# Kernel tuning notes

Hardware: AMD Instinct MI355X
Metric: run time of the kernel (lower is better)

## Reference

```python
import jax, jax.numpy as jnp
import numpy as np

B, A, EMBED, HIDDEN, PROJ = 256, 16, 1024, 1024, 256


def setup_inputs() -> dict:
    key = jax.random.key(0)
    k0, k1, k2 = jax.random.split(key, 3)
    return {
        "agent_embeddings": jax.random.normal(k0, (B, A, EMBED), dtype=jnp.float32),
        "w1": jax.random.normal(k1, (EMBED, HIDDEN), dtype=jnp.float32) * (1.0 / np.sqrt(EMBED)),
        "b1": jnp.zeros((HIDDEN,), dtype=jnp.float32),
        "w2": jax.random.normal(k2, (HIDDEN, PROJ), dtype=jnp.float32) * (1.0 / np.sqrt(HIDDEN)),
        "b2": jnp.zeros((PROJ,), dtype=jnp.float32),
        "log_scale": jnp.asarray(0.0, dtype=jnp.float32),  # log(init_logit_scale=1.0)
        "logit_bias": jnp.asarray(0.0, dtype=jnp.float32),
    }


def reference(agent_embeddings, w1, b1, w2, b2, log_scale, logit_bias):
    b, a, d = agent_embeddings.shape
    n = b * a
    x = agent_embeddings.reshape(n, d)
    # MLP projector: Linear -> GELU (exact, torch default) -> [dropout=identity at eval] -> Linear
    h = jax.nn.gelu(x @ w1 + b1, approximate=False)
    p = h @ w2 + b2  # [N, proj_dim]
    z = p / jnp.linalg.norm(p, axis=-1, keepdims=True)
    # cosine similarity logits, scaled + biased
    logits = (z @ z.T) * jnp.exp(log_scale) + logit_bias  # [N, N]
    # block-diagonal labels: 1 iff same batch element
    ids = jnp.arange(n) // a
    m1 = jnp.where(ids[:, None] == ids[None, :], 1.0, -1.0)  # 2*labels - 1
    loglik = jax.nn.log_sigmoid(m1 * logits)
    loss = jnp.mean(-jnp.sum(loglik, axis=-1))
    embeddings = z.reshape(b, a, -1)
    return embeddings, loss, logits
```

## Files before the change

### kernel.cpp

```cpp
#include <hip/hip_runtime.h>
#include <math.h>


#define NTOK 4096
#define DEMB 1024
#define DHID 1024
#define DPRJ 256

typedef __attribute__((ext_vector_type(8))) short bf16x8;
typedef __attribute__((ext_vector_type(4))) float f32x4;

typedef __attribute__((address_space(3))) void lds_void_t;
typedef __attribute__((address_space(1))) const void gbl_void_t;

static __device__ __forceinline__ void glds16(const void* g, void* l) {
    __builtin_amdgcn_global_load_lds((gbl_void_t*)g, (lds_void_t*)l, 16, 0, 0);
}

static __device__ __forceinline__ void split2(float v, ushort* h, ushort* l) {
    const uint u = __float_as_uint(v);
    *h = (ushort)(u >> 16);
    const float r = v - __uint_as_float(u & 0xffff0000u);
    *l = (ushort)(__float_as_uint(r) >> 16);
}
static __device__ __forceinline__ float gelu_fast(float v) {
    const float x  = v * 0.70710678118654752440f;
    const float ax = fabsf(x);
    const float t  = 1.0f / (1.0f + 0.3275911f * ax);
    const float poly = t * (0.254829592f + t * (-0.284496736f + t * (1.421413741f
                     + t * (-1.453152027f + t * 1.061405429f))));
    const float erf_ax = 1.0f - poly * __expf(-ax * ax);
    return 0.5f * v * (1.0f + copysignf(erf_ax, x));
}
static __device__ __forceinline__ float log_sigmoid_fast(float x) {
    return fminf(x, 0.0f) - __logf(1.0f + __expf(-fabsf(x)));
}

__global__ __launch_bounds__(256)
void k_cvt_T(const float* __restrict__ W, ushort* __restrict__ WtH,
             ushort* __restrict__ WtL, int K, int N)
{
    __shared__ float tile[32][33];
    const int tn0 = blockIdx.x * 32;
    const int tk0 = blockIdx.y * 32;
    const int tr = threadIdx.x >> 5;
    const int tc = threadIdx.x & 31;
#pragma unroll
    for (int p = 0; p < 4; ++p)
        tile[tr + 8 * p][tc] = W[(size_t)(tk0 + tr + 8 * p) * N + tn0 + tc];
    __syncthreads();
#pragma unroll
    for (int p = 0; p < 4; ++p) {
        const int n = tr + 8 * p;
        ushort h, l;
        split2(tile[tc][n], &h, &l);
        WtH[(size_t)(tn0 + n) * K + tk0 + tc] = h;
        WtL[(size_t)(tn0 + n) * K + tk0 + tc] = l;
    }
}

__global__ __launch_bounds__(256)
void k_cvt_X(const float* __restrict__ X, ushort* __restrict__ Xh,
             ushort* __restrict__ Xl)
{
    const size_t idx = ((size_t)blockIdx.x * 256 + threadIdx.x) * 8;
    const float4 v0 = *(const float4*)(X + idx);
    const float4 v1 = *(const float4*)(X + idx + 4);
    const float vv[8] = {v0.x, v0.y, v0.z, v0.w, v1.x, v1.y, v1.z, v1.w};
    uint4 hv, lv;
#pragma unroll
    for (int e = 0; e < 8; ++e)
        split2(vv[e], (ushort*)&hv + e, (ushort*)&lv + e);
    *(uint4*)(Xh + idx) = hv;
    *(uint4*)(Xl + idx) = lv;
}

__global__ __launch_bounds__(512, 1)
void k_gemm1(const ushort* __restrict__ Xh, const ushort* __restrict__ Xl,
             const ushort* __restrict__ W1tH, const ushort* __restrict__ W1tL,
             const float* __restrict__ B1, int bm0,
             ushort* __restrict__ Hh, ushort* __restrict__ Hl)
{
    __shared__ __align__(16) ushort sm[49152];
    ushort* Ah = sm;
    ushort* Al = sm + 16384;
    ushort* Bh = sm + 32768;
    ushort* Bl = sm + 40960;

    const int t = threadIdx.x, lane = t & 63, w = t >> 6;
    const int wr = w >> 2, wc = w & 3;
    const int bmr = blockIdx.x * 128;
    const int bn  = blockIdx.y * 64;
    const int kb = lane >> 4, lr = lane & 15;

    f32x4 acc[4];
#pragma unroll
    for (int i = 0; i < 4; ++i) acc[i] = (f32x4){0.f, 0.f, 0.f, 0.f};

    for (int ph = 0; ph < 8; ++ph) {
        const int ko = ph * 128;
        if (ph) __syncthreads();
#pragma unroll
        for (int q = 0; q < 4; ++q) {
            const int row = w * 16 + q * 4 + (lane >> 4);
            const int gck = (lane & 15) ^ (row & 15);
            const size_t ga = (size_t)(bmr + row) * DEMB + ko + (gck << 3);
            const int lo = (w * 16 + q * 4) * 128;
            glds16(Xh + ga, Ah + lo);
            glds16(Xl + ga, Al + lo);
        }
#pragma unroll
        for (int q = 0; q < 2; ++q) {
            const int row = w * 8 + q * 4 + (lane >> 4);
            const int gck = (lane & 15) ^ (row & 15);
            const size_t gb = (size_t)(bn + row) * DEMB + ko + (gck << 3);
            const int lo = (w * 8 + q * 4) * 128;
            glds16(W1tH + gb, Bh + lo);
            glds16(W1tL + gb, Bl + lo);
        }
        __syncthreads();
#pragma unroll
        for (int ks = 0; ks < 4; ++ks) {
            const int g = ks * 4 + kb;
            const int colL = wc * 16 + lr;
            const int ob = colL * 128 + ((g ^ (colL & 15)) << 3);
            const bf16x8 bh = *(const bf16x8*)(Bh + ob);
            const bf16x8 bl = *(const bf16x8*)(Bl + ob);
#pragma unroll
            for (int i = 0; i < 4; ++i) {
                const int rowL = wr * 64 + i * 16 + lr;
                const int oa = rowL * 128 + ((g ^ (rowL & 15)) << 3);
                const bf16x8 ah = *(const bf16x8*)(Ah + oa);
                const bf16x8 al = *(const bf16x8*)(Al + oa);
                acc[i] = __builtin_amdgcn_mfma_f32_16x16x32_bf16(ah, bh, acc[i], 0, 0, 0);
                acc[i] = __builtin_amdgcn_mfma_f32_16x16x32_bf16(ah, bl, acc[i], 0, 0, 0);
                acc[i] = __builtin_amdgcn_mfma_f32_16x16x32_bf16(al, bh, acc[i], 0, 0, 0);
            }
        }
    }

    const int col = bn + wc * 16 + lr;
    const float b = B1[col];
#pragma unroll
    for (int i = 0; i < 4; ++i) {
#pragma unroll
        for (int e = 0; e < 4; ++e) {
            const int row = bm0 + bmr + wr * 64 + i * 16 + kb * 4 + e;
            const float g = gelu_fast(acc[i][e] + b);
            ushort h, l;
            split2(g, &h, &l);
            Hh[(size_t)row * DHID + col] = h;
            Hl[(size_t)row * DHID + col] = l;
        }
    }
}

__global__ __launch_bounds__(512, 1)
void k_gemm2(const ushort* __restrict__ Hh, const ushort* __restrict__ Hl,
             const ushort* __restrict__ W2tH, const ushort* __restrict__ W2tL,
             float* __restrict__ P)
{
    __shared__ __align__(16) ushort sm[49152];
    ushort* Ah = sm;
    ushort* Al = sm + 16384;
    ushort* Bh = sm + 32768;
    ushort* Bl = sm + 40960;

    const int t = threadIdx.x, lane = t & 63, w = t >> 6;
    const int wr = w >> 2, wc = w & 3;
    const int bmr = blockIdx.x * 128;
    const int bn  = blockIdx.y * 64;
    const int k0  = blockIdx.z * 512;
    const int kb = lane >> 4, lr = lane & 15;

    f32x4 acc[4];
#pragma unroll
    for (int i = 0; i < 4; ++i) acc[i] = (f32x4){0.f, 0.f, 0.f, 0.f};

    for (int ph = 0; ph < 4; ++ph) {
        const int ko = k0 + ph * 128;
        if (ph) __syncthreads();
#pragma unroll
        for (int q = 0; q < 4; ++q) {
            const int row = w * 16 + q * 4 + (lane >> 4);
            const int gck = (lane & 15) ^ (row & 15);
            const size_t ga = (size_t)(bmr + row) * DHID + ko + (gck << 3);
            const int lo = (w * 16 + q * 4) * 128;
            glds16(Hh + ga, Ah + lo);
            glds16(Hl + ga, Al + lo);
        }
#pragma unroll
        for (int q = 0; q < 2; ++q) {
            const int row = w * 8 + q * 4 + (lane >> 4);
            const int gck = (lane & 15) ^ (row & 15);
            const size_t gb = (size_t)(bn + row) * DHID + ko + (gck << 3);
            const int lo = (w * 8 + q * 4) * 128;
            glds16(W2tH + gb, Bh + lo);
            glds16(W2tL + gb, Bl + lo);
        }
        __syncthreads();
#pragma unroll
        for (int ks = 0; ks < 4; ++ks) {
            const int g = ks * 4 + kb;
            const int colL = wc * 16 + lr;
            const int ob = colL * 128 + ((g ^ (colL & 15)) << 3);
            const bf16x8 bh = *(const bf16x8*)(Bh + ob);
            const bf16x8 bl = *(const bf16x8*)(Bl + ob);
#pragma unroll
            for (int i = 0; i < 4; ++i) {
                const int rowL = wr * 64 + i * 16 + lr;
                const int oa = rowL * 128 + ((g ^ (rowL & 15)) << 3);
                const bf16x8 ah = *(const bf16x8*)(Ah + oa);
                const bf16x8 al = *(const bf16x8*)(Al + oa);
                acc[i] = __builtin_amdgcn_mfma_f32_16x16x32_bf16(ah, bh, acc[i], 0, 0, 0);
                acc[i] = __builtin_amdgcn_mfma_f32_16x16x32_bf16(ah, bl, acc[i], 0, 0, 0);
                acc[i] = __builtin_amdgcn_mfma_f32_16x16x32_bf16(al, bh, acc[i], 0, 0, 0);
            }
        }
    }

    float* Pz = P + (size_t)blockIdx.z * NTOK * DPRJ;
    const int col = bn + wc * 16 + lr;
#pragma unroll
    for (int i = 0; i < 4; ++i) {
#pragma unroll
        for (int e = 0; e < 4; ++e) {
            const int row = bmr + wr * 64 + i * 16 + kb * 4 + e;
            Pz[(size_t)row * DPRJ + col] = acc[i][e];
        }
    }
}

__global__ __launch_bounds__(256)
void k_norm(const float* __restrict__ P, const float* __restrict__ B2,
            float* __restrict__ Zo, ushort* __restrict__ Zbh,
            ushort* __restrict__ Zbl)
{
    const int r = blockIdx.x;
    const int c = threadIdx.x;

    const float v = P[(size_t)r * DPRJ + c]
                  + P[(size_t)NTOK * DPRJ + (size_t)r * DPRJ + c] + B2[c];
    float ss = v * v;
#pragma unroll
    for (int o = 32; o > 0; o >>= 1) ss += __shfl_down(ss, o);
    __shared__ float wsum[4];
    if ((c & 63) == 0) wsum[c >> 6] = ss;
    __syncthreads();
    const float tot = wsum[0] + wsum[1] + wsum[2] + wsum[3];
    const float z = v / sqrtf(tot);
    Zo[(size_t)r * DPRJ + c] = z;
    ushort h, l;
    split2(z, &h, &l);
    Zbh[(size_t)r * DPRJ + c] = h;
    Zbl[(size_t)r * DPRJ + c] = l;
}

__global__ __launch_bounds__(512, 1)
void k_gemm3(const ushort* __restrict__ Zbh, const ushort* __restrict__ Zbl,
             const float* __restrict__ LS, const float* __restrict__ LB,
             float* __restrict__ Lg, float* __restrict__ partial)
{
    __shared__ __align__(16) ushort sm[65536];
    ushort* Ah = sm;
    ushort* Al = sm + 16384;
    ushort* Bh = sm + 32768;
    ushort* Bl = sm + 49152;

    const int t = threadIdx.x, lane = t & 63, w = t >> 6;
    const int wr = w >> 2, wc = w & 3;
    const int bm = blockIdx.x * 128, bn = blockIdx.y * 128;
    const int kb = lane >> 4, lr = lane & 15;
    const int srow0 = w * 16;

    f32x4 acc[4][2];
#pragma unroll
    for (int i = 0; i < 4; ++i)
#pragma unroll
        for (int j = 0; j < 2; ++j) acc[i][j] = (f32x4){0.f, 0.f, 0.f, 0.f};

    float lsum = 0.0f;

#pragma unroll
    for (int ph = 0; ph < 2; ++ph) {
        const int ko = ph * 128;
        if (ph) __syncthreads();
#pragma unroll
        for (int q = 0; q < 4; ++q) {
            const int row = srow0 + q * 4 + (lane >> 4);
            const int gck = (lane & 15) ^ (row & 15);
            const size_t ga = (size_t)(bm + row) * DPRJ + ko + (gck << 3);
            const size_t gb = (size_t)(bn + row) * DPRJ + ko + (gck << 3);
            const int lo = (srow0 + q * 4) * 128;
            glds16(Zbh + ga, Ah + lo);
            glds16(Zbl + ga, Al + lo);
            glds16(Zbh + gb, Bh + lo);
            glds16(Zbl + gb, Bl + lo);
        }
        __syncthreads();
#pragma unroll
        for (int ks = 0; ks < 4; ++ks) {
            const int g = ks * 4 + kb;
            bf16x8 bhf[2], blf[2];
#pragma unroll
            for (int j = 0; j < 2; ++j) {
                const int col = wc * 32 + j * 16 + lr;
                const int o = col * 128 + ((g ^ (col & 15)) << 3);
                bhf[j] = *(const bf16x8*)(Bh + o);
                blf[j] = *(const bf16x8*)(Bl + o);
            }
#pragma unroll
            for (int i = 0; i < 4; ++i) {
                const int row = wr * 64 + i * 16 + lr;
                const int o = row * 128 + ((g ^ (row & 15)) << 3);
                const bf16x8 ah = *(const bf16x8*)(Ah + o);
                const bf16x8 al = *(const bf16x8*)(Al + o);
#pragma unroll
                for (int j = 0; j < 2; ++j) {
                    acc[i][j] = __builtin_amdgcn_mfma_f32_16x16x32_bf16(ah, bhf[j], acc[i][j], 0, 0, 0);
                    acc[i][j] = __builtin_amdgcn_mfma_f32_16x16x32_bf16(ah, blf[j], acc[i][j], 0, 0, 0);
                    acc[i][j] = __builtin_amdgcn_mfma_f32_16x16x32_bf16(al, bhf[j], acc[i][j], 0, 0, 0);
                }
            }
        }
    }

    const float scale = __expf(LS[0]);
    const float lbias = LB[0];

    __syncthreads();
    float* fT = (float*)sm;
#pragma unroll
    for (int j = 0; j < 2; ++j) {
        const int col = bn + wc * 32 + j * 16 + lr;
        const int cid = col >> 4;
#pragma unroll
        for (int i = 0; i < 4; ++i) {
#pragma unroll
            for (int e = 0; e < 4; ++e) {
                const int rloc = wr * 64 + i * 16 + kb * 4 + e;
                const float lg = fmaf(acc[i][j][e], scale, lbias);
                fT[rloc * 132 + (wc * 32 + j * 16 + lr)] = lg;
                const float x = (((bm + rloc) >> 4) == cid) ? lg : -lg;
                lsum += log_sigmoid_fast(x);
            }
        }
    }
    __syncthreads();

#pragma unroll
    for (int q = 0; q < 32; ++q) {
        const int e = q * 512 + t;
        const int row = e >> 7, c = e & 127;
        Lg[(size_t)(bm + row) * NTOK + bn + c] = fT[row * 132 + c];
    }

#pragma unroll
    for (int o = 32; o > 0; o >>= 1) lsum += __shfl_down(lsum, o);
    __shared__ float wsum[8];
    if (lane == 0) wsum[w] = lsum;
    __syncthreads();
    if (t == 0) {
        float s = 0.f;
#pragma unroll
        for (int i = 0; i < 8; ++i) s += wsum[i];
        partial[blockIdx.y * gridDim.x + blockIdx.x] = s;
    }
}

__global__ __launch_bounds__(256)
void k_finalize(const float* __restrict__ partial, float* __restrict__ loss_out)
{
    const int t = threadIdx.x;
    double s = (double)partial[t] + (double)partial[t + 256]
             + (double)partial[t + 512] + (double)partial[t + 768];
#pragma unroll
    for (int o = 32; o > 0; o >>= 1) s += __shfl_down(s, o);
    __shared__ double ws4[4];
    if ((t & 63) == 0) ws4[t >> 6] = s;
    __syncthreads();
    if (t == 0)
        loss_out[0] = (float)(-(ws4[0] + ws4[1] + ws4[2] + ws4[3]) / (double)NTOK);
}

extern "C" void kernel_launch(void* const* d_in, const int* in_sizes, int n_in,
                              void* d_out, int out_size, void* d_ws, size_t ws_size,
                              hipStream_t stream)
{
    const float* X  = (const float*)d_in[0];
    const float* W1 = (const float*)d_in[1];
    const float* B1 = (const float*)d_in[2];
    const float* W2 = (const float*)d_in[3];
    const float* B2 = (const float*)d_in[4];
    const float* LS = (const float*)d_in[5];
    const float* LB = (const float*)d_in[6];

    float* out  = (float*)d_out;
    float* Zo   = out;
    float* loss = out + (size_t)NTOK * DPRJ;
    float* Lg   = loss + 1;

    char* ws = (char*)d_ws;
    ushort* Hh   = (ushort*)(ws);
    ushort* Hl   = (ushort*)(ws + 8388608);
    ushort* Xsh  = (ushort*)(ws + 16777216);
    ushort* Xsl  = (ushort*)(ws + 20971520);
    float*  P    = (float*) (ws + 16777216);
    ushort* W1tH = (ushort*)(ws + 25165824);
    ushort* W1tL = (ushort*)(ws + 27262976);
    ushort* Zbh  = (ushort*)(ws + 25165824);
    ushort* Zbl  = (ushort*)(ws + 27262976);
    ushort* W2tH = (ushort*)(ws + 29360128);
    ushort* W2tL = (ushort*)(ws + 29884416);
    float*  part = (float*) (ws + 30408704);

    k_cvt_T <<<dim3(32, 32),   256, 0, stream>>>(W1, W1tH, W1tL, DEMB, DHID);
    k_cvt_T <<<dim3(8, 32),    256, 0, stream>>>(W2, W2tH, W2tL, DHID, DPRJ);
    k_cvt_X <<<dim3(1024),     256, 0, stream>>>(X, Xsh, Xsl);
    k_gemm1 <<<dim3(16, 16),   512, 0, stream>>>(Xsh, Xsl, W1tH, W1tL, B1, 0, Hh, Hl);
    k_cvt_X <<<dim3(1024),     256, 0, stream>>>(X + (size_t)2048 * DEMB, Xsh, Xsl);
    k_gemm1 <<<dim3(16, 16),   512, 0, stream>>>(Xsh, Xsl, W1tH, W1tL, B1, 2048, Hh, Hl);

    k_gemm2 <<<dim3(32, 4, 2), 512, 0, stream>>>(Hh, Hl, W2tH, W2tL, P);
    k_norm  <<<dim3(4096),     256, 0, stream>>>(P, B2, Zo, Zbh, Zbl);
    k_gemm3 <<<dim3(32, 32),   512, 0, stream>>>(Zbh, Zbl, LS, LB, Lg, part);
    k_finalize<<<1, 256, 0, stream>>>(part, loss);
}
```

Baseline: 208.1 us.

## Double-buffer GEMM1/GEMM2 LDS stages, shrink K tiles, raise occupancy, merge weight conversion

GEMM1 and GEMM2 switch from single-buffered 128-wide K stages to double-buffered 64-wide stages, so the global-to-LDS loads for the next stage can overlap the MFMA work on the current one. The LDS footprint per block stays the same, and launch bounds now allow two blocks per CU. GEMM3 uses 64-wide K stages with half the LDS and four blocks per CU, and writes logits out through LDS in two halves. The two weight conversion launches become a single kernel. The risks are more barriers per K step and higher register pressure under the tighter launch bounds.

```diff
diff --git a/kernel.cpp b/kernel.cpp
--- a/kernel.cpp
+++ b/kernel.cpp
@@ -37,12 +37,23 @@
 }
 
 __global__ __launch_bounds__(256)
-void k_cvt_T(const float* __restrict__ W, ushort* __restrict__ WtH,
-             ushort* __restrict__ WtL, int K, int N)
+void k_cvt_W(const float* __restrict__ W1, ushort* __restrict__ W1tH,
+             ushort* __restrict__ W1tL, const float* __restrict__ W2,
+             ushort* __restrict__ W2tH, ushort* __restrict__ W2tL)
 {
     __shared__ float tile[32][33];
-    const int tn0 = blockIdx.x * 32;
-    const int tk0 = blockIdx.y * 32;
+    int id = blockIdx.x;
+    const float* W;
+    ushort *WtH, *WtL;
+    int K, N, tn0, tk0;
+    if (id < 1024) {
+        W = W1; WtH = W1tH; WtL = W1tL; K = DEMB; N = DHID;
+        tn0 = (id & 31) * 32; tk0 = (id >> 5) * 32;
+    } else {
+        id -= 1024;
+        W = W2; WtH = W2tH; WtL = W2tL; K = DHID; N = DPRJ;
+        tn0 = (id & 7) * 32; tk0 = (id >> 3) * 32;
+    }
     const int tr = threadIdx.x >> 5;
     const int tc = threadIdx.x & 31;
 #pragma unroll
@@ -75,68 +86,71 @@
     *(uint4*)(Xl + idx) = lv;
 }
 
-__global__ __launch_bounds__(512, 1)
+#define G1B 24576
+__global__ __launch_bounds__(512, 2)
 void k_gemm1(const ushort* __restrict__ Xh, const ushort* __restrict__ Xl,
              const ushort* __restrict__ W1tH, const ushort* __restrict__ W1tL,
              const float* __restrict__ B1, int bm0,
              ushort* __restrict__ Hh, ushort* __restrict__ Hl)
 {
-    __shared__ __align__(16) ushort sm[49152];
-    ushort* Ah = sm;
-    ushort* Al = sm + 16384;
-    ushort* Bh = sm + 32768;
-    ushort* Bl = sm + 40960;
-
+    __shared__ __align__(16) ushort sm[2 * G1B];
     const int t = threadIdx.x, lane = t & 63, w = t >> 6;
     const int wr = w >> 2, wc = w & 3;
-    const int bmr = blockIdx.x * 128;
-    const int bn  = blockIdx.y * 64;
+    const int bmr = blockIdx.x * 128, bn = blockIdx.y * 64;
     const int kb = lane >> 4, lr = lane & 15;
+    const int srow = lane >> 3, sck = lane & 7;
 
     f32x4 acc[4];
 #pragma unroll
     for (int i = 0; i < 4; ++i) acc[i] = (f32x4){0.f, 0.f, 0.f, 0.f};
 
-    for (int ph = 0; ph < 8; ++ph) {
-        const int ko = ph * 128;
-        if (ph) __syncthreads();
-#pragma unroll
-        for (int q = 0; q < 4; ++q) {
-            const int row = w * 16 + q * 4 + (lane >> 4);
-            const int gck = (lane & 15) ^ (row & 15);
-            const size_t ga = (size_t)(bmr + row) * DEMB + ko + (gck << 3);
-            const int lo = (w * 16 + q * 4) * 128;
-            glds16(Xh + ga, Ah + lo);
-            glds16(Xl + ga, Al + lo);
-        }
-#pragma unroll
-        for (int q = 0; q < 2; ++q) {
-            const int row = w * 8 + q * 4 + (lane >> 4);
-            const int gck = (lane & 15) ^ (row & 15);
-            const size_t gb = (size_t)(bn + row) * DEMB + ko + (gck << 3);
-            const int lo = (w * 8 + q * 4) * 128;
-            glds16(W1tH + gb, Bh + lo);
-            glds16(W1tL + gb, Bl + lo);
-        }
-        __syncthreads();
-#pragma unroll
-        for (int ks = 0; ks < 4; ++ks) {
+#define G1_STAGE(buf, ko)                                                   \
+    {                                                                       \
+        _Pragma("unroll")                                                   \
+        for (int q = 0; q < 2; ++q) {                                       \
+            const int row = w * 16 + q * 8 + srow;                          \
+            const int gck = sck ^ (row & 7);                                \
+            const size_t ga = (size_t)(bmr + row) * DEMB + (ko) + (gck << 3);\
+            const int lo = (w * 16 + q * 8) * 64;                           \
+            glds16(Xh + ga, (buf) + lo);                                    \
+            glds16(Xl + ga, (buf) + 8192 + lo);                             \
+        }                                                                   \
+        {                                                                   \
+            const int row = w * 8 + srow;                                   \
+            const int gck = sck ^ (row & 7);                                \
+            const size_t gb = (size_t)(bn + row) * DEMB + (ko) + (gck << 3);\
+            const int lo = (w * 8) * 64;                                    \
+            glds16(W1tH + gb, (buf) + 16384 + lo);                          \
+            glds16(W1tL + gb, (buf) + 20480 + lo);                          \
+        }                                                                   \
+    }
+
+    G1_STAGE(sm, 0);
+    __syncthreads();
+    int co = 0;
+    for (int ph = 0; ph < 16; ++ph) {
+        if (ph < 15) { G1_STAGE(sm + (co ^ G1B), (ph + 1) * 64); }
+        const ushort* cb = sm + co;
+#pragma unroll
+        for (int ks = 0; ks < 2; ++ks) {
             const int g = ks * 4 + kb;
-            const int colL = wc * 16 + lr;
-            const int ob = colL * 128 + ((g ^ (colL & 15)) << 3);
-            const bf16x8 bh = *(const bf16x8*)(Bh + ob);
-            const bf16x8 bl = *(const bf16x8*)(Bl + ob);
+            const int col = wc * 16 + lr;
+            const int ob = col * 64 + ((g ^ (col & 7)) << 3);
+            const bf16x8 bh = *(const bf16x8*)(cb + 16384 + ob);
+            const bf16x8 bl = *(const bf16x8*)(cb + 20480 + ob);
 #pragma unroll
             for (int i = 0; i < 4; ++i) {
-                const int rowL = wr * 64 + i * 16 + lr;
-                const int oa = rowL * 128 + ((g ^ (rowL & 15)) << 3);
-                const bf16x8 ah = *(const bf16x8*)(Ah + oa);
-                const bf16x8 al = *(const bf16x8*)(Al + oa);
+                const int row = wr * 64 + i * 16 + lr;
+                const int oa = row * 64 + ((g ^ (row & 7)) << 3);
+                const bf16x8 ah = *(const bf16x8*)(cb + oa);
+                const bf16x8 al = *(const bf16x8*)(cb + 8192 + oa);
                 acc[i] = __builtin_amdgcn_mfma_f32_16x16x32_bf16(ah, bh, acc[i], 0, 0, 0);
                 acc[i] = __builtin_amdgcn_mfma_f32_16x16x32_bf16(ah, bl, acc[i], 0, 0, 0);
                 acc[i] = __builtin_amdgcn_mfma_f32_16x16x32_bf16(al, bh, acc[i], 0, 0, 0);
             }
         }
+        __syncthreads();
+        co ^= G1B;
     }
 
     const int col = bn + wc * 16 + lr;
@@ -155,68 +169,70 @@
     }
 }
 
-__global__ __launch_bounds__(512, 1)
+__global__ __launch_bounds__(512, 2)
 void k_gemm2(const ushort* __restrict__ Hh, const ushort* __restrict__ Hl,
              const ushort* __restrict__ W2tH, const ushort* __restrict__ W2tL,
              float* __restrict__ P)
 {
-    __shared__ __align__(16) ushort sm[49152];
-    ushort* Ah = sm;
-    ushort* Al = sm + 16384;
-    ushort* Bh = sm + 32768;
-    ushort* Bl = sm + 40960;
-
+    __shared__ __align__(16) ushort sm[2 * G1B];
     const int t = threadIdx.x, lane = t & 63, w = t >> 6;
     const int wr = w >> 2, wc = w & 3;
-    const int bmr = blockIdx.x * 128;
-    const int bn  = blockIdx.y * 64;
-    const int k0  = blockIdx.z * 512;
+    const int bmr = blockIdx.x * 128, bn = blockIdx.y * 64;
+    const int k0 = blockIdx.z * 512;
     const int kb = lane >> 4, lr = lane & 15;
+    const int srow = lane >> 3, sck = lane & 7;
 
     f32x4 acc[4];
 #pragma unroll
     for (int i = 0; i < 4; ++i) acc[i] = (f32x4){0.f, 0.f, 0.f, 0.f};
 
-    for (int ph = 0; ph < 4; ++ph) {
-        const int ko = k0 + ph * 128;
-        if (ph) __syncthreads();
-#pragma unroll
-        for (int q = 0; q < 4; ++q) {
-            const int row = w * 16 + q * 4 + (lane >> 4);
-            const int gck = (lane & 15) ^ (row & 15);
-            const size_t ga = (size_t)(bmr + row) * DHID + ko + (gck << 3);
-            const int lo = (w * 16 + q * 4) * 128;
-            glds16(Hh + ga, Ah + lo);
-            glds16(Hl + ga, Al + lo);
-        }
-#pragma unroll
-        for (int q = 0; q < 2; ++q) {
-            const int row = w * 8 + q * 4 + (lane >> 4);
-            const int gck = (lane & 15) ^ (row & 15);
-            const size_t gb = (size_t)(bn + row) * DHID + ko + (gck << 3);
-            const int lo = (w * 8 + q * 4) * 128;
-            glds16(W2tH + gb, Bh + lo);
-            glds16(W2tL + gb, Bl + lo);
-        }
-        __syncthreads();
-#pragma unroll
-        for (int ks = 0; ks < 4; ++ks) {
+#define G2_STAGE(buf, ko)                                                   \
+    {                                                                       \
+        _Pragma("unroll")                                                   \
+        for (int q = 0; q < 2; ++q) {                                       \
+            const int row = w * 16 + q * 8 + srow;                          \
+            const int gck = sck ^ (row & 7);                                \
+            const size_t ga = (size_t)(bmr + row) * DHID + (ko) + (gck << 3);\
+            const int lo = (w * 16 + q * 8) * 64;                           \
+            glds16(Hh + ga, (buf) + lo);                                    \
+            glds16(Hl + ga, (buf) + 8192 + lo);                             \
+        }                                                                   \
+        {                                                                   \
+            const int row = w * 8 + srow;                                   \
+            const int gck = sck ^ (row & 7);                                \
+            const size_t gb = (size_t)(bn + row) * DHID + (ko) + (gck << 3);\
+            const int lo = (w * 8) * 64;                                    \
+            glds16(W2tH + gb, (buf) + 16384 + lo);                          \
+            glds16(W2tL + gb, (buf) + 20480 + lo);                          \
+        }                                                                   \
+    }
+
+    G2_STAGE(sm, k0);
+    __syncthreads();
+    int co = 0;
+    for (int ph = 0; ph < 8; ++ph) {
+        if (ph < 7) { G2_STAGE(sm + (co ^ G1B), k0 + (ph + 1) * 64); }
+        const ushort* cb = sm + co;
+#pragma unroll
+        for (int ks = 0; ks < 2; ++ks) {
             const int g = ks * 4 + kb;
-            const int colL = wc * 16 + lr;
-            const int ob = colL * 128 + ((g ^ (colL & 15)) << 3);
-            const bf16x8 bh = *(const bf16x8*)(Bh + ob);
-            const bf16x8 bl = *(const bf16x8*)(Bl + ob);
+            const int col = wc * 16 + lr;
+            const int ob = col * 64 + ((g ^ (col & 7)) << 3);
+            const bf16x8 bh = *(const bf16x8*)(cb + 16384 + ob);
+            const bf16x8 bl = *(const bf16x8*)(cb + 20480 + ob);
 #pragma unroll
             for (int i = 0; i < 4; ++i) {
-                const int rowL = wr * 64 + i * 16 + lr;
-                const int oa = rowL * 128 + ((g ^ (rowL & 15)) << 3);
-                const bf16x8 ah = *(const bf16x8*)(Ah + oa);
-                const bf16x8 al = *(const bf16x8*)(Al + oa);
+                const int row = wr * 64 + i * 16 + lr;
+                const int oa = row * 64 + ((g ^ (row & 7)) << 3);
+                const bf16x8 ah = *(const bf16x8*)(cb + oa);
+                const bf16x8 al = *(const bf16x8*)(cb + 8192 + oa);
                 acc[i] = __builtin_amdgcn_mfma_f32_16x16x32_bf16(ah, bh, acc[i], 0, 0, 0);
                 acc[i] = __builtin_amdgcn_mfma_f32_16x16x32_bf16(ah, bl, acc[i], 0, 0, 0);
                 acc[i] = __builtin_amdgcn_mfma_f32_16x16x32_bf16(al, bh, acc[i], 0, 0, 0);
             }
         }
+        __syncthreads();
+        co ^= G1B;
     }
 
     float* Pz = P + (size_t)blockIdx.z * NTOK * DPRJ;
@@ -256,22 +272,22 @@
     Zbl[(size_t)r * DPRJ + c] = l;
 }
 
-__global__ __launch_bounds__(512, 1)
+__global__ __launch_bounds__(512, 4)
 void k_gemm3(const ushort* __restrict__ Zbh, const ushort* __restrict__ Zbl,
              const float* __restrict__ LS, const float* __restrict__ LB,
              float* __restrict__ Lg, float* __restrict__ partial)
 {
-    __shared__ __align__(16) ushort sm[65536];
+    __shared__ __align__(16) ushort sm[32768];
     ushort* Ah = sm;
-    ushort* Al = sm + 16384;
-    ushort* Bh = sm + 32768;
-    ushort* Bl = sm + 49152;
+    ushort* Al = sm + 8192;
+    ushort* Bh = sm + 16384;
+    ushort* Bl = sm + 24576;
 
     const int t = threadIdx.x, lane = t & 63, w = t >> 6;
     const int wr = w >> 2, wc = w & 3;
     const int bm = blockIdx.x * 128, bn = blockIdx.y * 128;
     const int kb = lane >> 4, lr = lane & 15;
-    const int srow0 = w * 16;
+    const int srow = lane >> 3, sck = lane & 7;
 
     f32x4 acc[4][2];
 #pragma unroll
@@ -279,19 +295,16 @@
 #pragma unroll
         for (int j = 0; j < 2; ++j) acc[i][j] = (f32x4){0.f, 0.f, 0.f, 0.f};
 
-    float lsum = 0.0f;
-
-#pragma unroll
-    for (int ph = 0; ph < 2; ++ph) {
-        const int ko = ph * 128;
+    for (int ph = 0; ph < 4; ++ph) {
+        const int ko = ph * 64;
         if (ph) __syncthreads();
 #pragma unroll
-        for (int q = 0; q < 4; ++q) {
-            const int row = srow0 + q * 4 + (lane >> 4);
-            const int gck = (lane & 15) ^ (row & 15);
+        for (int q = 0; q < 2; ++q) {
+            const int row = w * 16 + q * 8 + srow;
+            const int gck = sck ^ (row & 7);
             const size_t ga = (size_t)(bm + row) * DPRJ + ko + (gck << 3);
             const size_t gb = (size_t)(bn + row) * DPRJ + ko + (gck << 3);
-            const int lo = (srow0 + q * 4) * 128;
+            const int lo = (w * 16 + q * 8) * 64;
             glds16(Zbh + ga, Ah + lo);
             glds16(Zbl + ga, Al + lo);
             glds16(Zbh + gb, Bh + lo);
@@ -299,20 +312,20 @@
         }
         __syncthreads();
 #pragma unroll
-        for (int ks = 0; ks < 4; ++ks) {
+        for (int ks = 0; ks < 2; ++ks) {
             const int g = ks * 4 + kb;
             bf16x8 bhf[2], blf[2];
 #pragma unroll
             for (int j = 0; j < 2; ++j) {
                 const int col = wc * 32 + j * 16 + lr;
-                const int o = col * 128 + ((g ^ (col & 15)) << 3);
+                const int o = col * 64 + ((g ^ (col & 7)) << 3);
                 bhf[j] = *(const bf16x8*)(Bh + o);
                 blf[j] = *(const bf16x8*)(Bl + o);
             }
 #pragma unroll
             for (int i = 0; i < 4; ++i) {
                 const int row = wr * 64 + i * 16 + lr;
-                const int o = row * 128 + ((g ^ (row & 15)) << 3);
+                const int o = row * 64 + ((g ^ (row & 7)) << 3);
                 const bf16x8 ah = *(const bf16x8*)(Ah + o);
                 const bf16x8 al = *(const bf16x8*)(Al + o);
 #pragma unroll
@@ -328,8 +341,7 @@
     const float scale = __expf(LS[0]);
     const float lbias = LB[0];
 
-    __syncthreads();
-    float* fT = (float*)sm;
+    float lsum = 0.0f;
 #pragma unroll
     for (int j = 0; j < 2; ++j) {
         const int col = bn + wc * 32 + j * 16 + lr;
@@ -338,21 +350,39 @@
         for (int i = 0; i < 4; ++i) {
 #pragma unroll
             for (int e = 0; e < 4; ++e) {
-                const int rloc = wr * 64 + i * 16 + kb * 4 + e;
+                const int row = bm + wr * 64 + i * 16 + kb * 4 + e;
                 const float lg = fmaf(acc[i][j][e], scale, lbias);
-                fT[rloc * 132 + (wc * 32 + j * 16 + lr)] = lg;
-                const float x = (((bm + rloc) >> 4) == cid) ? lg : -lg;
+                const float x = ((row >> 4) == cid) ? lg : -lg;
                 lsum += log_sigmoid_fast(x);
             }
         }
     }
-    __syncthreads();
-
-#pragma unroll
-    for (int q = 0; q < 32; ++q) {
-        const int e = q * 512 + t;
-        const int row = e >> 7, c = e & 127;
-        Lg[(size_t)(bm + row) * NTOK + bn + c] = fT[row * 132 + c];
+
+    float* fT = (float*)sm;
+#pragma unroll
+    for (int p = 0; p < 2; ++p) {
+        __syncthreads();
+        if (wr == p) {
+#pragma unroll
+            for (int j = 0; j < 2; ++j) {
+#pragma unroll
+                for (int i = 0; i < 4; ++i) {
+#pragma unroll
+                    for (int e = 0; e < 4; ++e) {
+                        const int rloc = i * 16 + kb * 4 + e;
+                        fT[rloc * 132 + (wc * 32 + j * 16 + lr)]
+                            = fmaf(acc[i][j][e], scale, lbias);
+                    }
+                }
+            }
+        }
+        __syncthreads();
+#pragma unroll
+        for (int q = 0; q < 16; ++q) {
+            const int e = q * 512 + t;
+            const int row = e >> 7, c = e & 127;
+            Lg[(size_t)(bm + p * 64 + row) * NTOK + bn + c] = fT[row * 132 + c];
+        }
     }
 
 #pragma unroll
@@ -414,8 +444,7 @@
     ushort* W2tL = (ushort*)(ws + 29884416);
     float*  part = (float*) (ws + 30408704);
 
-    k_cvt_T <<<dim3(32, 32),   256, 0, stream>>>(W1, W1tH, W1tL, DEMB, DHID);
-    k_cvt_T <<<dim3(8, 32),    256, 0, stream>>>(W2, W2tH, W2tL, DHID, DPRJ);
+    k_cvt_W <<<dim3(1280),     256, 0, stream>>>(W1, W1tH, W1tL, W2, W2tH, W2tL);
     k_cvt_X <<<dim3(1024),     256, 0, stream>>>(X, Xsh, Xsl);
     k_gemm1 <<<dim3(16, 16),   512, 0, stream>>>(Xsh, Xsl, W1tH, W1tL, B1, 0, Hh, Hl);
     k_cvt_X <<<dim3(1024),     256, 0, stream>>>(X + (size_t)2048 * DEMB, Xsh, Xsl);
```

After: 199.9 us. -3.9%, faster.
